# Performance work log

Hardware: AMD Instinct MI355X
Metric: run time of the kernel (lower is better)

Reference implementation:

```python
import jax, jax.numpy as jnp
import numpy as np

N_COLS = 4096
N_ROWS = 4096
H = 64          # args.hidden1
S = 2           # per-edge supp feature count (cv_supp/vc_supp dim 0)
S_VO = 2        # vo_supp feature dim
S_CO = 2        # co_supp feature dim
EDGE_DENSITY = 0.03


def setup_inputs() -> dict:
    key = jax.random.key(0)
    ks = jax.random.split(key, 20)
    col_hidden = jax.random.normal(ks[0], (N_COLS, H), jnp.float32)
    row_hidden = jax.random.normal(ks[1], (N_ROWS, H), jnp.float32)
    obj_hidden = jax.random.normal(ks[2], (1, H), jnp.float32)
    # sparse bipartite adjacency encoded in supp[0] != 0 (as in the TF code)
    mask = jax.random.bernoulli(ks[3], EDGE_DENSITY, (N_ROWS, N_COLS))
    cv_supp = jax.random.normal(ks[4], (S, N_ROWS, N_COLS), jnp.float32) * mask[None]
    vc_supp = jnp.transpose(cv_supp, (0, 2, 1))  # [S, ncols, nrows]
    vo_supp = jax.random.normal(ks[5], (N_COLS, S_VO), jnp.float32)
    co_supp = jax.random.normal(ks[6], (N_ROWS, S_CO), jnp.float32)
    w = 0.05
    W_vo = jax.random.normal(ks[7], (2 * H, H), jnp.float32) * w
    W_oc = jax.random.normal(ks[8], (2 * H, H), jnp.float32) * w
    W_vc = jax.random.normal(ks[9], (2 * H, H), jnp.float32) * w
    W_co = jax.random.normal(ks[10], (2 * H, H), jnp.float32) * w
    W_ov = jax.random.normal(ks[11], (2 * H, H), jnp.float32) * w
    W_cv = jax.random.normal(ks[12], (2 * H, H), jnp.float32) * w
    # attention scorer nets: Dense(concat_dim -> 1) + sigmoid
    w_attn_vo = jax.random.normal(ks[13], (2 * H + S_VO, 1), jnp.float32) * 0.1
    b_attn_vo = jnp.zeros((), jnp.float32)
    w_attn_co = jax.random.normal(ks[14], (2 * H + S_CO, 1), jnp.float32) * 0.1
    b_attn_co = jnp.zeros((), jnp.float32)
    # pairwise attn nets decomposed into [col | supp | row] weight slices
    w_cv_col = jax.random.normal(ks[15], (H,), jnp.float32) * 0.1
    w_cv_supp = jax.random.normal(ks[16], (S,), jnp.float32) * 0.1
    w_cv_row = jax.random.normal(ks[17], (H,), jnp.float32) * 0.1
    b_cv = jnp.zeros((), jnp.float32)
    w_vc_row = jax.random.normal(ks[18], (H,), jnp.float32) * 0.1
    w_vc_supp = jax.random.normal(ks[19], (S,), jnp.float32) * 0.1
    w_vc_col = jax.random.normal(jax.random.fold_in(key, 99), (H,), jnp.float32) * 0.1
    b_vc = jnp.zeros((), jnp.float32)
    return dict(col_hidden=col_hidden, row_hidden=row_hidden, obj_hidden=obj_hidden,
                cv_supp=cv_supp, vc_supp=vc_supp, vo_supp=vo_supp, co_supp=co_supp,
                W_vo=W_vo, W_oc=W_oc, W_vc=W_vc, W_co=W_co, W_ov=W_ov, W_cv=W_cv,
                w_attn_vo=w_attn_vo, b_attn_vo=b_attn_vo,
                w_attn_co=w_attn_co, b_attn_co=b_attn_co,
                w_cv_col=w_cv_col, w_cv_supp=w_cv_supp, w_cv_row=w_cv_row, b_cv=b_cv,
                w_vc_row=w_vc_row, w_vc_supp=w_vc_supp, w_vc_col=w_vc_col, b_vc=b_vc)


def _forward(col_hidden, row_hidden, obj_hidden, cv_supp, vc_supp, vo_supp, co_supp,
             W_vo, W_oc, W_vc, W_co, W_ov, W_cv,
             w_attn_vo, b_attn_vo, w_attn_co, b_attn_co,
             w_cv_col, w_cv_supp, w_cv_row, b_cv,
             w_vc_row, w_vc_supp, w_vc_col, b_vc):
    act = jax.nn.relu
    ncols, nrows = col_hidden.shape[0], row_hidden.shape[0]
    # ---- v -> o: attend over all columns, update obj node ----
    vo_in = jnp.concatenate([col_hidden, vo_supp,
                             jnp.broadcast_to(obj_hidden, (ncols, H))], axis=1)
    a_vo = jax.nn.sigmoid(vo_in @ w_attn_vo + b_attn_vo)          # [ncols, 1]
    v_o_out = a_vo.T @ col_hidden                                  # [1, H]
    obj = act(jnp.concatenate([obj_hidden, v_o_out], axis=1) @ W_vo)
    # ---- v -> c: per-row ragged neighbor attention, vectorized via masked pairwise scores ----
    nbr_cv = cv_supp[0] != 0                                       # [nrows, ncols]
    logits_cv = ((row_hidden @ w_cv_row)[:, None]
                 + (col_hidden @ w_cv_col)[None, :]
                 + jnp.einsum('snc,s->nc', cv_supp, w_cv_supp) + b_cv)
    score_cv = jnp.where(nbr_cv, jax.nn.sigmoid(logits_cv), 0.0)   # [nrows, ncols]
    v_out = score_cv @ col_hidden                                  # [nrows, H]
    o_c_out = act(jnp.concatenate([jnp.broadcast_to(obj, (nrows, H)), row_hidden], axis=1) @ W_oc)
    row_next = act(jnp.concatenate([o_c_out, v_out], axis=1) @ W_vc)
    # ---- c -> o ----
    co_in = jnp.concatenate([row_next, co_supp,
                             jnp.broadcast_to(obj, (nrows, H))], axis=1)
    a_co = jax.nn.sigmoid(co_in @ w_attn_co + b_attn_co)           # [nrows, 1]
    c_o_out = a_co.T @ row_next                                    # [1, H]
    obj = act(jnp.concatenate([obj, c_o_out], axis=1) @ W_co)
    # ---- c -> v ----
    nbr_vc = vc_supp[0] != 0                                       # [ncols, nrows]
    logits_vc = ((col_hidden @ w_vc_col)[:, None]
                 + (row_next @ w_vc_row)[None, :]
                 + jnp.einsum('scn,s->cn', vc_supp, w_vc_supp) + b_vc)
    score_vc = jnp.where(nbr_vc, jax.nn.sigmoid(logits_vc), 0.0)   # [ncols, nrows]
    c_out = score_vc @ row_next                                    # [ncols, H]
    o_v_out = act(jnp.concatenate([jnp.broadcast_to(obj, (ncols, H)), col_hidden], axis=1) @ W_ov)
    col_next = act(jnp.concatenate([o_v_out, c_out], axis=1) @ W_cv)
    return col_next, row_next, obj


def reference(col_hidden, row_hidden, obj_hidden, cv_supp, vc_supp, vo_supp, co_supp,
              W_vo, W_oc, W_vc, W_co, W_ov, W_cv,
              w_attn_vo, b_attn_vo, w_attn_co, b_attn_co,
              w_cv_col, w_cv_supp, w_cv_row, b_cv,
              w_vc_row, w_vc_supp, w_vc_col, b_vc):
    col_next, row_next, obj = _forward(
        col_hidden, row_hidden, obj_hidden, cv_supp, vc_supp, vo_supp, co_supp,
        W_vo, W_oc, W_vc, W_co, W_ov, W_cv,
        w_attn_vo, b_attn_vo, w_attn_co, b_attn_co,
        w_cv_col, w_cv_supp, w_cv_row, b_cv,
        w_vc_row, w_vc_supp, w_vc_col, b_vc)
    # original layer also passes the supp tensors through unchanged
    return (col_next, row_next, obj, cv_supp, vc_supp, vo_supp, co_supp)
```

## Files before the change

### kernel.cpp

```cpp
#include <hip/hip_runtime.h>
#include <math.h>

typedef float f4 __attribute__((ext_vector_type(4)));

#define PLANE (4096*4096)

#define OUT_COL 0
#define OUT_ROW 262144
#define OUT_OBJ 524288
#define OUT_CV  524352
#define OUT_VC  34078784
#define OUT_VO  67633216
#define OUT_CO  67641408

#define WS_VO_P 0
#define WS_CO_P 4096
#define WS_OBJ1 8192
#define WS_RDCV 8256
#define WS_CDCV 12352
#define WS_RDVC 16448
#define WS_CDVC 20544
#define WS_PART 24640

__device__ __forceinline__ float sigf(float x) {
    return 1.0f / (1.0f + __expf(-x));
}

__device__ __forceinline__ float enc_sj(float s, int j) {
    return __uint_as_float((__float_as_uint(s) & 0xFFFFFF00u) | (unsigned)j);
}

__device__ __forceinline__ void attn_body64(
    int blk, int t, const float* __restrict__ X, const float* __restrict__ supp,
    const float* __restrict__ obj, const float* __restrict__ wat,
    const float* __restrict__ bat, float* __restrict__ accP,
    const float* __restrict__ wextra, float* __restrict__ dextra,
    float* sA, float* sAcc)
{
    const int w = t >> 6, lane = t & 63;
    if (t < 64) {
        const int i = blk * 64 + t;
        float od = 0.f;
        for (int h = 0; h < 64; ++h) od += obj[h] * wat[66 + h];
        float x = bat[0] + od + supp[i*2] * wat[64] + supp[i*2+1] * wat[65];
        const f4* Xr = (const f4*)(X + i*64);
        f4 xd = 0.f, dd = 0.f;
        #pragma unroll
        for (int q = 0; q < 16; ++q) {
            f4 xv = Xr[q];
            xd += xv * ((const f4*)wat)[q];
            if (wextra) dd += xv * ((const f4*)wextra)[q];
        }
        x += xd.x + xd.y + xd.z + xd.w;
        if (dextra) dextra[i] = dd.x + dd.y + dd.z + dd.w;
        sA[t] = sigf(x);
        sAcc[t] = 0.f;
    }
    __syncthreads();
    float partial = 0.f;
    const int jbase = blk * 64 + w * 16;
    for (int j = 0; j < 16; ++j)
        partial += sA[w*16 + j] * X[(jbase + j)*64 + lane];
    atomicAdd(&sAcc[lane], partial);
    __syncthreads();
    if (t < 64) accP[blk*64 + t] = sAcc[t];
}

__global__ __launch_bounds__(256) void k_front(
    const float* __restrict__ col_hidden, const float* __restrict__ row_hidden,
    const float* __restrict__ w_cv_col, const float* __restrict__ w_vc_col,
    const float* __restrict__ w_cv_row,
    float* __restrict__ cdcv, float* __restrict__ cdvc, float* __restrict__ rdcv,
    const float* __restrict__ vo_supp, const float* __restrict__ co_supp,
    float* __restrict__ out_vo, float* __restrict__ out_co,
    const float* __restrict__ obj_hidden, const float* __restrict__ w_attn_vo,
    const float* __restrict__ b_attn_vo, float* __restrict__ voP)
{
    __shared__ float sA[64];
    __shared__ float sAcc[64];
    const int t = threadIdx.x;
    if (blockIdx.x < 3072) {
        const int gw = blockIdx.x * 4 + (t >> 6);
        const int lane = t & 63;
        const int which = gw >> 12;
        const int row = gw & 4095;
        const float* x; const float* w; float* dst;
        if (which == 0)      { x = col_hidden; w = w_cv_col; dst = cdcv; }
        else if (which == 1) { x = col_hidden; w = w_vc_col; dst = cdvc; }
        else                 { x = row_hidden; w = w_cv_row; dst = rdcv; }
        float v = x[row * 64 + lane] * w[lane];
        #pragma unroll
        for (int off = 32; off; off >>= 1) v += __shfl_down(v, off, 64);
        if (lane == 0) dst[row] = v;
        return;
    }
    if (blockIdx.x < 3088) {
        const int idx = (blockIdx.x - 3072) * 256 + t;
        if (idx < 2048) ((f4*)out_vo)[idx] = ((const f4*)vo_supp)[idx];
        else            ((f4*)out_co)[idx - 2048] = ((const f4*)co_supp)[idx - 2048];
        return;
    }
    attn_body64(blockIdx.x - 3088, t, col_hidden, vo_supp, obj_hidden,
                w_attn_vo, b_attn_vo, voP, nullptr, nullptr, sA, sAcc);
}

__global__ __launch_bounds__(256) void k_attn(
    const float* __restrict__ X, const float* __restrict__ supp,
    const float* __restrict__ obj, const float* __restrict__ wat,
    const float* __restrict__ bat, float* __restrict__ accP,
    const float* __restrict__ wextra, float* __restrict__ dextra)
{
    __shared__ float sA[64];
    __shared__ float sAcc[64];
    attn_body64(blockIdx.x, threadIdx.x, X, supp, obj, wat, bat, accP,
                wextra, dextra, sA, sAcc);
}

__global__ __launch_bounds__(256, 4) void k_big(
    const float* __restrict__ supp0, const float* __restrict__ supp1,
    const float* __restrict__ Bm,
    const float* __restrict__ rdot, const float* __restrict__ cdot,
    const float* __restrict__ wsup, const float* __restrict__ bias,
    float* __restrict__ part, float* __restrict__ pass0, float* __restrict__ pass1,
    const float* __restrict__ objL, const float* __restrict__ objRp,
    const float* __restrict__ Wobj, float* __restrict__ objDst)
{
    __shared__ __align__(16) float list[64][33];
    const int t = threadIdx.x;

    if (blockIdx.x == 2048) {
        float* red = &list[0][0];
        if (t < 64) {
            float r = 0.f;
            for (int b = 0; b < 64; ++b) r += objRp[b*64 + t];
            red[t] = r;
        }
        __syncthreads();
        if (t < 64) {
            float acc = 0.f;
            for (int k = 0; k < 64; ++k) acc += objL[k] * Wobj[k*64 + t];
            for (int k = 0; k < 64; ++k) acc += red[k] * Wobj[(64+k)*64 + t];
            objDst[t] = fmaxf(acc, 0.f);
        }
        return;
    }

    const int bi = blockIdx.x >> 5;
    const int bj = blockIdx.x & 31;
    const int i0 = bi * 64;
    const int jt0 = bj * 128;
    const int w = t >> 6, lane = t & 63;
    const int hi = lane >> 5;
    const int sl = lane & 31;
    const float w0 = wsup[0], w1 = wsup[1], bv = bias[0];

    {
        const f4 cd = *(const f4*)(cdot + jt0 + sl * 4);
        #pragma unroll 2
        for (int q = 0; q < 8; ++q) {
            const int row = 8*q + 2*w + hi;
            const size_t g = (size_t)(i0 + row) * 4096 + jt0 + sl * 4;
            f4 a0 = *(const f4*)(supp0 + g);
            f4 a1 = *(const f4*)(supp1 + g);
            __builtin_nontemporal_store(a0, (f4*)(pass0 + g));
            __builtin_nontemporal_store(a1, (f4*)(pass1 + g));
            const float rd = rdot[i0 + row];
            f4 lg = rd + cd + w0 * a0 + w1 * a1 + bv;
            const int c0 = (a0.x != 0.f), c1 = (a0.y != 0.f);
            const int c2 = (a0.z != 0.f), c3 = (a0.w != 0.f);
            const int m = c0 + c1 + c2 + c3;
            int sum = m;
            #pragma unroll
            for (int d = 1; d < 32; d <<= 1) {
                int x = __shfl_up(sum, d, 32);
                if (sl >= d) sum += x;
            }
            int pos = sum - m;
            float* Lrow = &list[row][0];
            if (c0) { if (pos < 31) Lrow[pos] = enc_sj(sigf(lg.x), sl*4 + 0); ++pos; }
            if (c1) { if (pos < 31) Lrow[pos] = enc_sj(sigf(lg.y), sl*4 + 1); ++pos; }
            if (c2) { if (pos < 31) Lrow[pos] = enc_sj(sigf(lg.z), sl*4 + 2); ++pos; }
            if (c3) { if (pos < 31) Lrow[pos] = enc_sj(sigf(lg.w), sl*4 + 3); ++pos; }
            if (sl == 31) Lrow[31] = __int_as_float(sum < 31 ? sum : 31);
        }
    }
    asm volatile("s_waitcnt lgkmcnt(0)" ::: "memory");
    __builtin_amdgcn_sched_barrier(0);

    {
        const int ri  = lane >> 2;
        const int hq  = lane & 3;
        const int row = 8*(ri >> 1) + 2*w + (ri & 1);
        const float* Lrow = &list[row][0];
        const int n = __float_as_int(Lrow[31]);
        f4 acc0 = 0.f, acc1 = 0.f, acc2 = 0.f, acc3 = 0.f;
        for (int k = 0; k < n; ++k) {
            const unsigned u = __float_as_uint(Lrow[k]);
            const int j = (int)(u & 0x7Fu);
            const float s = __uint_as_float(u & 0xFFFFFF00u);
            const f4* Br = (const f4*)(Bm + (size_t)(jt0 + j) * 64 + hq * 16);
            acc0 += s * Br[0];
            acc1 += s * Br[1];
            acc2 += s * Br[2];
            acc3 += s * Br[3];
        }
        float* pb = part + (size_t)bj * 262144 + (size_t)(i0 + row) * 64 + hq * 16;
        *(f4*)(pb + 0)  = acc0;
        *(f4*)(pb + 4)  = acc1;
        *(f4*)(pb + 8)  = acc2;
        *(f4*)(pb + 12) = acc3;
    }
}

__global__ __launch_bounds__(256) void k_mlp2(
    const float* __restrict__ objx, const float* __restrict__ base,
    const float* __restrict__ W1, const float* __restrict__ part,
    const float* __restrict__ W2, float* __restrict__ dst)
{
    __shared__ float mid[4][64];
    __shared__ float accsP[4][256];
    __shared__ float accs[4][64];
    const int t = threadIdx.x, w = t >> 6, h = t & 63, lane = t & 63;
    const int nbase = blockIdx.x * 4;
    f4 v = 0.f;
    #pragma unroll
    for (int j = w; j < 32; j += 4)
        v += *(const f4*)(part + (size_t)j * 262144 + blockIdx.x * 256 + lane * 4);
    *(f4*)&accsP[w][lane * 4] = v;
    float m = 0.f;
    for (int k = 0; k < 64; ++k) m += objx[k] * W1[k*64 + h];
    for (int k = 0; k < 64; ++k) m += base[(nbase + w)*64 + k] * W1[(64+k)*64 + h];
    mid[w][h] = fmaxf(m, 0.f);
    __syncthreads();
    accs[t >> 6][t & 63] = accsP[0][t] + accsP[1][t] + accsP[2][t] + accsP[3][t];
    __syncthreads();
    float o = 0.f;
    for (int k = 0; k < 64; ++k) o += mid[w][k] * W2[k*64 + h];
    for (int k = 0; k < 64; ++k) o += accs[w][k] * W2[(64+k)*64 + h];
    dst[(nbase + w)*64 + h] = fmaxf(o, 0.f);
}

extern "C" void kernel_launch(void* const* d_in, const int* in_sizes, int n_in,
                              void* d_out, int out_size, void* d_ws, size_t ws_size,
                              hipStream_t stream)
{
    const float* col_hidden = (const float*)d_in[0];
    const float* row_hidden = (const float*)d_in[1];
    const float* obj_hidden = (const float*)d_in[2];
    const float* cv_supp    = (const float*)d_in[3];
    const float* vc_supp    = (const float*)d_in[4];
    const float* vo_supp    = (const float*)d_in[5];
    const float* co_supp    = (const float*)d_in[6];
    const float* W_vo       = (const float*)d_in[7];
    const float* W_oc       = (const float*)d_in[8];
    const float* W_vc       = (const float*)d_in[9];
    const float* W_co       = (const float*)d_in[10];
    const float* W_ov       = (const float*)d_in[11];
    const float* W_cv       = (const float*)d_in[12];
    const float* w_attn_vo  = (const float*)d_in[13];
    const float* b_attn_vo  = (const float*)d_in[14];
    const float* w_attn_co  = (const float*)d_in[15];
    const float* b_attn_co  = (const float*)d_in[16];
    const float* w_cv_col   = (const float*)d_in[17];
    const float* w_cv_supp  = (const float*)d_in[18];
    const float* w_cv_row   = (const float*)d_in[19];
    const float* b_cv       = (const float*)d_in[20];
    const float* w_vc_row   = (const float*)d_in[21];
    const float* w_vc_supp  = (const float*)d_in[22];
    const float* w_vc_col   = (const float*)d_in[23];
    const float* b_vc       = (const float*)d_in[24];

    float* out = (float*)d_out;
    float* ws  = (float*)d_ws;

    k_front<<<3152, 256, 0, stream>>>(col_hidden, row_hidden, w_cv_col, w_vc_col, w_cv_row,
                                      ws + WS_CDCV, ws + WS_CDVC, ws + WS_RDCV,
                                      vo_supp, co_supp, out + OUT_VO, out + OUT_CO,
                                      obj_hidden, w_attn_vo, b_attn_vo, ws + WS_VO_P);
    k_big<<<2049, 256, 0, stream>>>(cv_supp, cv_supp + PLANE, col_hidden,
                                    ws + WS_RDCV, ws + WS_CDCV, w_cv_supp, b_cv,
                                    ws + WS_PART, out + OUT_CV, out + OUT_CV + PLANE,
                                    obj_hidden, ws + WS_VO_P, W_vo, ws + WS_OBJ1);
    k_mlp2<<<1024, 256, 0, stream>>>(ws + WS_OBJ1, row_hidden, W_oc, ws + WS_PART, W_vc,
                                     out + OUT_ROW);
    k_attn<<<64, 256, 0, stream>>>(out + OUT_ROW, co_supp, ws + WS_OBJ1, w_attn_co, b_attn_co,
                                   ws + WS_CO_P, w_vc_row, ws + WS_RDVC);
    k_big<<<2049, 256, 0, stream>>>(vc_supp, vc_supp + PLANE, out + OUT_ROW,
                                    ws + WS_CDVC, ws + WS_RDVC, w_vc_supp, b_vc,
                                    ws + WS_PART, out + OUT_VC, out + OUT_VC + PLANE,
                                    ws + WS_OBJ1, ws + WS_CO_P, W_co, out + OUT_OBJ);
    k_mlp2<<<1024, 256, 0, stream>>>(out + OUT_OBJ, col_hidden, W_ov, ws + WS_PART, W_cv,
                                     out + OUT_COL);
}
```

Before: 582.5 us.

## Process full rows per wavefront in sparse aggregation, removing column-tile partial sums

Each wavefront now scans one full 4096-wide row, compacting nonzeros into a 256-entry LDS list with a 12-bit column index. It then accumulates the row's output directly, with lanes mapping to hidden units. This removes the 32-way partial-sum buffer and its reduction in k_mlp2, cutting workspace traffic and halving the grid. The risks are fewer blocks and lower parallelism per row, reduced sigmoid precision from 12 dropped mantissa bits, and silent truncation if a row has more than 256 nonzeros.

```diff
diff --git a/kernel.cpp b/kernel.cpp
--- a/kernel.cpp
+++ b/kernel.cpp
@@ -27,7 +27,7 @@
 }
 
 __device__ __forceinline__ float enc_sj(float s, int j) {
-    return __uint_as_float((__float_as_uint(s) & 0xFFFFFF00u) | (unsigned)j);
+    return __uint_as_float((__float_as_uint(s) & 0xFFFFF000u) | (unsigned)j);
 }
 
 __device__ __forceinline__ void attn_body64(
@@ -121,14 +121,14 @@
     const float* __restrict__ Bm,
     const float* __restrict__ rdot, const float* __restrict__ cdot,
     const float* __restrict__ wsup, const float* __restrict__ bias,
-    float* __restrict__ part, float* __restrict__ pass0, float* __restrict__ pass1,
+    float* __restrict__ vout, float* __restrict__ pass0, float* __restrict__ pass1,
     const float* __restrict__ objL, const float* __restrict__ objRp,
     const float* __restrict__ Wobj, float* __restrict__ objDst)
 {
-    __shared__ __align__(16) float list[64][33];
+    __shared__ __align__(16) float list[4][256];
     const int t = threadIdx.x;
 
-    if (blockIdx.x == 2048) {
+    if (blockIdx.x == 1024) {
         float* red = &list[0][0];
         if (t < 64) {
             float r = 0.f;
@@ -145,71 +145,52 @@
         return;
     }
 
-    const int bi = blockIdx.x >> 5;
-    const int bj = blockIdx.x & 31;
-    const int i0 = bi * 64;
-    const int jt0 = bj * 128;
     const int w = t >> 6, lane = t & 63;
-    const int hi = lane >> 5;
-    const int sl = lane & 31;
+    const int r = blockIdx.x * 4 + w;
     const float w0 = wsup[0], w1 = wsup[1], bv = bias[0];
-
-    {
-        const f4 cd = *(const f4*)(cdot + jt0 + sl * 4);
-        #pragma unroll 2
-        for (int q = 0; q < 8; ++q) {
-            const int row = 8*q + 2*w + hi;
-            const size_t g = (size_t)(i0 + row) * 4096 + jt0 + sl * 4;
-            f4 a0 = *(const f4*)(supp0 + g);
-            f4 a1 = *(const f4*)(supp1 + g);
-            __builtin_nontemporal_store(a0, (f4*)(pass0 + g));
-            __builtin_nontemporal_store(a1, (f4*)(pass1 + g));
-            const float rd = rdot[i0 + row];
-            f4 lg = rd + cd + w0 * a0 + w1 * a1 + bv;
-            const int c0 = (a0.x != 0.f), c1 = (a0.y != 0.f);
-            const int c2 = (a0.z != 0.f), c3 = (a0.w != 0.f);
-            const int m = c0 + c1 + c2 + c3;
-            int sum = m;
-            #pragma unroll
-            for (int d = 1; d < 32; d <<= 1) {
-                int x = __shfl_up(sum, d, 32);
-                if (sl >= d) sum += x;
-            }
-            int pos = sum - m;
-            float* Lrow = &list[row][0];
-            if (c0) { if (pos < 31) Lrow[pos] = enc_sj(sigf(lg.x), sl*4 + 0); ++pos; }
-            if (c1) { if (pos < 31) Lrow[pos] = enc_sj(sigf(lg.y), sl*4 + 1); ++pos; }
-            if (c2) { if (pos < 31) Lrow[pos] = enc_sj(sigf(lg.z), sl*4 + 2); ++pos; }
-            if (c3) { if (pos < 31) Lrow[pos] = enc_sj(sigf(lg.w), sl*4 + 3); ++pos; }
-            if (sl == 31) Lrow[31] = __int_as_float(sum < 31 ? sum : 31);
-        }
+    const float rd = rdot[r];
+    float* Lrow = &list[w][0];
+
+    int base = 0;
+    #pragma unroll 2
+    for (int c = 0; c < 16; ++c) {
+        const size_t g = (size_t)r * 4096 + c * 256 + lane * 4;
+        f4 a0 = *(const f4*)(supp0 + g);
+        f4 a1 = *(const f4*)(supp1 + g);
+        __builtin_nontemporal_store(a0, (f4*)(pass0 + g));
+        __builtin_nontemporal_store(a1, (f4*)(pass1 + g));
+        const f4 cd = *(const f4*)(cdot + c * 256 + lane * 4);
+        f4 lg = rd + cd + w0 * a0 + w1 * a1 + bv;
+        const int c0 = (a0.x != 0.f), c1 = (a0.y != 0.f);
+        const int c2 = (a0.z != 0.f), c3 = (a0.w != 0.f);
+        const int m = c0 + c1 + c2 + c3;
+        int sum = m;
+        #pragma unroll
+        for (int d = 1; d < 64; d <<= 1) {
+            int x = __shfl_up(sum, d, 64);
+            if (lane >= d) sum += x;
+        }
+        int pos = base + sum - m;
+        const int jb = c * 256 + lane * 4;
+        if (c0) { if (pos < 256) Lrow[pos] = enc_sj(sigf(lg.x), jb + 0); ++pos; }
+        if (c1) { if (pos < 256) Lrow[pos] = enc_sj(sigf(lg.y), jb + 1); ++pos; }
+        if (c2) { if (pos < 256) Lrow[pos] = enc_sj(sigf(lg.z), jb + 2); ++pos; }
+        if (c3) { if (pos < 256) Lrow[pos] = enc_sj(sigf(lg.w), jb + 3); ++pos; }
+        base += __shfl(sum, 63, 64);
     }
     asm volatile("s_waitcnt lgkmcnt(0)" ::: "memory");
     __builtin_amdgcn_sched_barrier(0);
 
-    {
-        const int ri  = lane >> 2;
-        const int hq  = lane & 3;
-        const int row = 8*(ri >> 1) + 2*w + (ri & 1);
-        const float* Lrow = &list[row][0];
-        const int n = __float_as_int(Lrow[31]);
-        f4 acc0 = 0.f, acc1 = 0.f, acc2 = 0.f, acc3 = 0.f;
-        for (int k = 0; k < n; ++k) {
-            const unsigned u = __float_as_uint(Lrow[k]);
-            const int j = (int)(u & 0x7Fu);
-            const float s = __uint_as_float(u & 0xFFFFFF00u);
-            const f4* Br = (const f4*)(Bm + (size_t)(jt0 + j) * 64 + hq * 16);
-            acc0 += s * Br[0];
-            acc1 += s * Br[1];
-            acc2 += s * Br[2];
-            acc3 += s * Br[3];
-        }
-        float* pb = part + (size_t)bj * 262144 + (size_t)(i0 + row) * 64 + hq * 16;
-        *(f4*)(pb + 0)  = acc0;
-        *(f4*)(pb + 4)  = acc1;
-        *(f4*)(pb + 8)  = acc2;
-        *(f4*)(pb + 12) = acc3;
-    }
+    const int n = base < 256 ? base : 256;
+    float acc = 0.f;
+    #pragma unroll 4
+    for (int k = 0; k < n; ++k) {
+        const unsigned u = __float_as_uint(Lrow[k]);
+        const int j = (int)(u & 0xFFFu);
+        const float s = __uint_as_float(u & 0xFFFFF000u);
+        acc += s * Bm[(size_t)j * 64 + lane];
+    }
+    vout[(size_t)r * 64 + lane] = acc;
 }
 
 __global__ __launch_bounds__(256) void k_mlp2(
@@ -218,26 +199,19 @@
     const float* __restrict__ W2, float* __restrict__ dst)
 {
     __shared__ float mid[4][64];
-    __shared__ float accsP[4][256];
     __shared__ float accs[4][64];
-    const int t = threadIdx.x, w = t >> 6, h = t & 63, lane = t & 63;
-    const int nbase = blockIdx.x * 4;
-    f4 v = 0.f;
-    #pragma unroll
-    for (int j = w; j < 32; j += 4)
-        v += *(const f4*)(part + (size_t)j * 262144 + blockIdx.x * 256 + lane * 4);
-    *(f4*)&accsP[w][lane * 4] = v;
+    const int t = threadIdx.x, w = t >> 6, h = t & 63;
+    const int n = blockIdx.x * 4 + w;
+    accs[w][h] = part[(size_t)n * 64 + h];
     float m = 0.f;
     for (int k = 0; k < 64; ++k) m += objx[k] * W1[k*64 + h];
-    for (int k = 0; k < 64; ++k) m += base[(nbase + w)*64 + k] * W1[(64+k)*64 + h];
+    for (int k = 0; k < 64; ++k) m += base[n*64 + k] * W1[(64+k)*64 + h];
     mid[w][h] = fmaxf(m, 0.f);
-    __syncthreads();
-    accs[t >> 6][t & 63] = accsP[0][t] + accsP[1][t] + accsP[2][t] + accsP[3][t];
     __syncthreads();
     float o = 0.f;
     for (int k = 0; k < 64; ++k) o += mid[w][k] * W2[k*64 + h];
     for (int k = 0; k < 64; ++k) o += accs[w][k] * W2[(64+k)*64 + h];
-    dst[(nbase + w)*64 + h] = fmaxf(o, 0.f);
+    dst[n*64 + h] = fmaxf(o, 0.f);
 }
 
 extern "C" void kernel_launch(void* const* d_in, const int* in_sizes, int n_in,
@@ -277,7 +251,7 @@
                                       ws + WS_CDCV, ws + WS_CDVC, ws + WS_RDCV,
                                       vo_supp, co_supp, out + OUT_VO, out + OUT_CO,
                                       obj_hidden, w_attn_vo, b_attn_vo, ws + WS_VO_P);
-    k_big<<<2049, 256, 0, stream>>>(cv_supp, cv_supp + PLANE, col_hidden,
+    k_big<<<1025, 256, 0, stream>>>(cv_supp, cv_supp + PLANE, col_hidden,
                                     ws + WS_RDCV, ws + WS_CDCV, w_cv_supp, b_cv,
                                     ws + WS_PART, out + OUT_CV, out + OUT_CV + PLANE,
                                     obj_hidden, ws + WS_VO_P, W_vo, ws + WS_OBJ1);
@@ -285,7 +259,7 @@
                                      out + OUT_ROW);
     k_attn<<<64, 256, 0, stream>>>(out + OUT_ROW, co_supp, ws + WS_OBJ1, w_attn_co, b_attn_co,
                                    ws + WS_CO_P, w_vc_row, ws + WS_RDVC);
-    k_big<<<2049, 256, 0, stream>>>(vc_supp, vc_supp + PLANE, out + OUT_ROW,
+    k_big<<<1025, 256, 0, stream>>>(vc_supp, vc_supp + PLANE, out + OUT_ROW,
                                     ws + WS_CDVC, ws + WS_RDVC, w_vc_supp, b_vc,
                                     ws + WS_PART, out + OUT_VC, out + OUT_VC + PLANE,
                                     ws + WS_OBJ1, ws + WS_CO_P, W_co, out + OUT_OBJ);
```

New measurement: 567.3 us. 2.6% less time.
